# Performance work log

Measured on AMD Instinct MI355X. Metric: run time of the kernel, lower is better.

Reference implementation:

```python
import jax, jax.numpy as jnp
import numpy as np

TAU = 0.07
MARGIN = 0.2
NUM_SPECIES = 64  # matches fill_max of species_ids


def _l2norm(x):
    return x / jnp.linalg.norm(x, axis=-1, keepdims=True)


def setup_inputs() -> dict:
    key = jax.random.key(0)
    k1, k2, k3 = jax.random.split(key, 3)
    B, D = 8192, 256
    species_embed = _l2norm(jax.random.normal(k1, (B, D), dtype=jnp.float32))
    text_embed = _l2norm(jax.random.normal(k2, (B, D), dtype=jnp.float32))
    species_ids = jax.random.randint(k3, (B,), 0, NUM_SPECIES, dtype=jnp.int32)
    return {"species_embed": species_embed, "text_embed": text_embed,
            "species_ids": species_ids}


def reference(species_embed, text_embed, species_ids):
    B = species_embed.shape[0]
    dtype = species_embed.dtype

    sim = species_embed @ text_embed.T                      # (B, B)
    same = species_ids[:, None] == species_ids[None, :]     # (B, B) bool, symmetric
    diag_sim = jnp.diagonal(sim)                            # (B,)

    # ---- intra-species symmetric InfoNCE (per-species CE, averaged over species)
    logits = sim / TAU
    neg_inf = jnp.finfo(dtype).min
    masked = jnp.where(same, logits, neg_inf)               # restrict to same-species cols
    diag_logit = diag_sim / TAU
    ce_v2t = jax.scipy.special.logsumexp(masked, axis=1) - diag_logit   # per-row CE
    ce_t2v = jax.scipy.special.logsumexp(masked.T, axis=1) - diag_logit # transpose: same mask is symmetric

    ones = jnp.ones((B,), dtype=dtype)
    counts = jax.ops.segment_sum(ones, species_ids, num_segments=NUM_SPECIES)          # group sizes
    seg_v2t = jax.ops.segment_sum(ce_v2t, species_ids, num_segments=NUM_SPECIES)
    seg_t2v = jax.ops.segment_sum(ce_t2v, species_ids, num_segments=NUM_SPECIES)
    valid_s = counts >= 2                                   # groups with <2 members skipped
    per_species = (seg_v2t + seg_t2v) / (2.0 * jnp.maximum(counts, 1.0))
    n_valid = jnp.maximum(jnp.sum(valid_s.astype(dtype)), 1.0)
    loss_infonce = jnp.sum(jnp.where(valid_s, per_species, 0.0)) / n_valid

    # ---- cross-species triplet (pos = mean same-species sim excl. self, neg = mean diff-species sim)
    same_f = same.astype(dtype)
    row_same_sum = jnp.sum(sim * same_f, axis=1)            # includes diagonal
    row_sum = jnp.sum(sim, axis=1)
    pos_cnt = jnp.sum(same_f, axis=1) - 1.0
    neg_cnt = B - jnp.sum(same_f, axis=1)
    pos_mean = (row_same_sum - diag_sim) / jnp.maximum(pos_cnt, 1.0)
    neg_mean = (row_sum - row_same_sum) / jnp.maximum(neg_cnt, 1.0)
    tri = jax.nn.relu(neg_mean - pos_mean + MARGIN)
    valid_i = (pos_cnt > 0) & (neg_cnt > 0)
    n_valid_i = jnp.maximum(jnp.sum(valid_i.astype(dtype)), 1.0)
    loss_triplet = jnp.sum(jnp.where(valid_i, tri, 0.0)) / n_valid_i

    return loss_infonce + loss_triplet
```

## Files before the change

kernel.cpp:

```cpp
#include <hip/hip_runtime.h>
#include <hip/hip_fp16.h>

#define TAU 0.07f
#define MARGIN 0.2f
#define NSPEC 64
#define BB 8192
#define DD 256

#define WS_SCALARS   0
#define WS_COUNTS    288
#define WS_OFFSETS   544
#define WS_LSEROW    1024
#define WS_LSECOL    33792
#define WS_TS        66560
#define WS_DIAG      132096
#define WS_MEMBER    164864
#define WS_T         197632
#define WS_TRI       198656
#define WS_ZERO_BYTES 132096

typedef _Float16 half8 __attribute__((ext_vector_type(8)));
typedef float float4v __attribute__((ext_vector_type(4)));
typedef unsigned int uint4v __attribute__((ext_vector_type(4)));

__device__ __forceinline__ uint4v pack8(float4 a, float4 b) {
  half8 h;
  h[0] = (_Float16)a.x; h[1] = (_Float16)a.y; h[2] = (_Float16)a.z; h[3] = (_Float16)a.w;
  h[4] = (_Float16)b.x; h[5] = (_Float16)b.y; h[6] = (_Float16)b.z; h[7] = (_Float16)b.w;
  return __builtin_bit_cast(uint4v, h);
}

__global__ void k1_all(const int* __restrict__ ids, int* counts_g, int* offsets_g,
                       int* memberList, float* scalars) {
  __shared__ int cnt[NSPEC];
  __shared__ int off[NSPEC];
  int tid = threadIdx.x;
  if (tid < NSPEC) cnt[tid] = 0;
  __syncthreads();
  int myS[8], myP[8];
  #pragma unroll
  for (int r = 0; r < 8; ++r) {
    int i = r * 1024 + tid;
    int s = ids[i];
    myS[r] = s;
    myP[r] = atomicAdd(&cnt[s], 1);
  }
  __syncthreads();
  if (tid < NSPEC) {
    int o = 0;
    for (int t = 0; t < NSPEC; ++t) o += (t < tid) ? cnt[t] : 0;
    off[tid] = o;
    offsets_g[tid] = o;
    int c = cnt[tid];
    counts_g[tid] = c;
    unsigned long long bv = __ballot(c >= 2);
    float nvi = (c >= 2 && c <= BB - 1) ? (float)c : 0.f;
    for (int o2 = 1; o2 < 64; o2 <<= 1) nvi += __shfl_xor(nvi, o2);
    if (tid == 0) {
      scalars[2] = (float)__popcll(bv);
      scalars[3] = nvi;
    }
  }
  __syncthreads();
  #pragma unroll
  for (int r = 0; r < 8; ++r) {
    int i = r * 1024 + tid;
    memberList[off[myS[r]] + myP[r]] = i;
  }
}

__global__ void k2_ts(const float* __restrict__ tx, const int* __restrict__ counts,
                      const int* __restrict__ offsets, const int* __restrict__ memberList,
                      float* Ts) {
  int s = blockIdx.x, r = blockIdx.y;
  int m = counts[s], g0 = offsets[s];
  int k0 = (m * r) >> 3, k1 = (m * (r + 1)) >> 3;
  if (k0 >= k1) return;
  int d = threadIdx.x;
  float acc = 0.f;
  for (int k = k0; k < k1; ++k) acc += tx[memberList[g0 + k] * DD + d];
  atomicAdd(&Ts[s * DD + d], acc);
}

__global__ void k2b_t(const float* __restrict__ Ts, float* T) {
  int d = threadIdx.x;
  float acc = 0.f;
  for (int s = 0; s < NSPEC; ++s) acc += Ts[s * DD + d];
  T[d] = acc;
}

__global__ void k4_rows(const float* __restrict__ sp, const float* __restrict__ tx,
                        const int* __restrict__ ids, const int* __restrict__ counts,
                        const float* __restrict__ Ts, const float* __restrict__ T,
                        float* diag, float* tri) {
  int gt = blockIdx.x * 256 + threadIdx.x;
  int i = gt >> 6, lane = gt & 63;
  float4 a = *reinterpret_cast<const float4*>(sp + i * DD + lane * 4);
  float4 b = *reinterpret_cast<const float4*>(tx + i * DD + lane * 4);
  float4 tv = *reinterpret_cast<const float4*>(T + lane * 4);
  int s = ids[i];
  int m = counts[s];
  float4 c = *reinterpret_cast<const float4*>(Ts + s * DD + lane * 4);
  float dDiag = a.x * b.x + a.y * b.y + a.z * b.z + a.w * b.w;
  float dT    = a.x * tv.x + a.y * tv.y + a.z * tv.z + a.w * tv.w;
  float dTs   = a.x * c.x + a.y * c.y + a.z * c.z + a.w * c.w;
  #pragma unroll
  for (int o = 1; o < 64; o <<= 1) {
    dDiag += __shfl_xor(dDiag, o);
    dT    += __shfl_xor(dT, o);
    dTs   += __shfl_xor(dTs, o);
  }
  if (lane == 0) {
    diag[i] = dDiag;
    float posMean = (dTs - dDiag) / fmaxf((float)(m - 1), 1.f);
    float negMean = (dT - dTs) / fmaxf((float)(BB - m), 1.f);
    float t = fmaxf(negMean - posMean + MARGIN, 0.f);
    tri[i] = (m >= 2 && m <= BB - 1) ? t : 0.f;
  }
}

__global__ void k5_lse(const float* __restrict__ sp, const float* __restrict__ tx,
                       const int* __restrict__ counts, const int* __restrict__ offsets,
                       const int* __restrict__ memberList,
                       float* lseRow, float* lseCol) {
  __shared__ uint4v lds5[1536];
  int s = blockIdx.x;
  int m = counts[s];
  int g0 = offsets[s];
  int tid = threadIdx.x;
  int lane = tid & 63, wv = tid >> 6;
  int quad = lane >> 4, cl = lane & 15;

  for (int rt = blockIdx.y; rt * 64 < m; rt += gridDim.y) {
    for (int ct = blockIdx.z; ct * 128 < m; ct += gridDim.z) {
      float4v acc[8];
      #pragma unroll
      for (int cf = 0; cf < 8; ++cf) acc[cf] = (float4v){0.f, 0.f, 0.f, 0.f};

      for (int kc = 0; kc < 4; ++kc) {
        __syncthreads();
        #pragma unroll
        for (int p = 0; p < 6; ++p) {
          int u = p * 256 + tid;
          int isB = u >= 512;
          int v = isB ? (u - 512) : u;
          int row = v >> 3;
          int sub = v & 7;
          int ksl = sub >> 2, q = sub & 3;
          int d0 = kc * 64 + ksl * 32 + q * 8;
          int idx = isB ? (ct * 128 + row) : (rt * 64 + row);
          uint4v val = (uint4v){0u, 0u, 0u, 0u};
          if (idx < m) {
            const float* src = (isB ? tx : sp) + memberList[g0 + idx] * DD + d0;
            float4 f0 = *reinterpret_cast<const float4*>(src);
            float4 f1 = *reinterpret_cast<const float4*>(src + 4);
            val = pack8(f0, f1);
          }
          int dst = isB ? (512 + (ksl * 128 + row) * 4 + q)
                        : ((ksl * 64 + row) * 4 + q);
          lds5[dst] = val;
        }
        __syncthreads();
        #pragma unroll
        for (int ksl = 0; ksl < 2; ++ksl) {
          half8 a = __builtin_bit_cast(half8, lds5[(ksl * 64 + wv * 16 + cl) * 4 + quad]);
          #pragma unroll
          for (int cf = 0; cf < 8; ++cf) {
            half8 b = __builtin_bit_cast(half8, lds5[512 + (ksl * 128 + cf * 16 + cl) * 4 + quad]);
            acc[cf] = __builtin_amdgcn_mfma_f32_16x16x32_f16(a, b, acc[cf], 0, 0, 0);
          }
        }
      }

      int riBase = rt * 64 + wv * 16 + quad * 4;
      float rowAcc[4] = {0.f, 0.f, 0.f, 0.f};
      #pragma unroll
      for (int cf = 0; cf < 8; ++cf) {
        int ci = ct * 128 + cf * 16 + cl;
        bool cv = ci < m;
        float colAcc = 0.f;
        #pragma unroll
        for (int reg = 0; reg < 4; ++reg) {
          bool rv = (riBase + reg) < m;
          float e = (rv && cv) ? __expf(acc[cf][reg] * (1.f / TAU)) : 0.f;
          rowAcc[reg] += e;
          colAcc += e;
        }
        colAcc += __shfl_xor(colAcc, 16);
        colAcc += __shfl_xor(colAcc, 32);
        if (quad == 0 && cv) atomicAdd(&lseCol[g0 + ci], colAcc);
      }
      #pragma unroll
      for (int reg = 0; reg < 4; ++reg) {
        float v = rowAcc[reg];
        v += __shfl_xor(v, 1);
        v += __shfl_xor(v, 2);
        v += __shfl_xor(v, 4);
        v += __shfl_xor(v, 8);
        if (cl == 0 && (riBase + reg) < m) atomicAdd(&lseRow[g0 + riBase + reg], v);
      }
    }
  }
}

__global__ void k6_info(const int* __restrict__ memberList, const int* __restrict__ ids,
                        const int* __restrict__ counts, const float* __restrict__ lseRow,
                        const float* __restrict__ lseCol, const float* __restrict__ diag,
                        const float* __restrict__ tri, float* scalars) {
  __shared__ float red[8];
  int g = blockIdx.x * blockDim.x + threadIdx.x;
  int i = memberList[g];
  int s = ids[i];
  int m = counts[s];
  float tt = tri[i];
  float term = 0.f;
  if (m >= 2) {
    term = (__logf(lseRow[g]) + __logf(lseCol[g]) - 2.f * diag[i] * (1.f / TAU)) /
           (2.f * (float)m);
  }
  #pragma unroll
  for (int o = 1; o < 64; o <<= 1) {
    term += __shfl_xor(term, o);
    tt += __shfl_xor(tt, o);
  }
  int wv = threadIdx.x >> 6, lane = threadIdx.x & 63;
  if (lane == 0) { red[wv] = term; red[4 + wv] = tt; }
  __syncthreads();
  if (threadIdx.x == 0) {
    atomicAdd(&scalars[1], red[0] + red[1] + red[2] + red[3]);
    atomicAdd(&scalars[0], red[4] + red[5] + red[6] + red[7]);
  }
}

__global__ void k7_final(const float* __restrict__ scalars, float* out) {
  out[0] = scalars[1] / fmaxf(scalars[2], 1.f) + scalars[0] / fmaxf(scalars[3], 1.f);
}

extern "C" void kernel_launch(void* const* d_in, const int* in_sizes, int n_in,
                              void* d_out, int out_size, void* d_ws, size_t ws_size,
                              hipStream_t stream) {
  const float* sp = (const float*)d_in[0];
  const float* tx = (const float*)d_in[1];
  const int* ids = (const int*)d_in[2];
  float* out = (float*)d_out;

  char* ws = (char*)d_ws;
  float* scalars = (float*)(ws + WS_SCALARS);
  int* counts = (int*)(ws + WS_COUNTS);
  int* offsets = (int*)(ws + WS_OFFSETS);
  float* lseRow = (float*)(ws + WS_LSEROW);
  float* lseCol = (float*)(ws + WS_LSECOL);
  float* Ts = (float*)(ws + WS_TS);
  float* diag = (float*)(ws + WS_DIAG);
  int* memberList = (int*)(ws + WS_MEMBER);
  float* T = (float*)(ws + WS_T);
  float* tri = (float*)(ws + WS_TRI);

  hipMemsetAsync(d_ws, 0, WS_ZERO_BYTES, stream);
  k1_all<<<1, 1024, 0, stream>>>(ids, counts, offsets, memberList, scalars);
  k2_ts<<<dim3(NSPEC, 8), 256, 0, stream>>>(tx, counts, offsets, memberList, Ts);
  k2b_t<<<1, 256, 0, stream>>>(Ts, T);
  k4_rows<<<BB / 4, 256, 0, stream>>>(sp, tx, ids, counts, Ts, T, diag, tri);
  k5_lse<<<dim3(NSPEC, 4, 2), 256, 0, stream>>>(sp, tx, counts, offsets, memberList,
                                                lseRow, lseCol);
  k6_info<<<32, 256, 0, stream>>>(memberList, ids, counts, lseRow, lseCol, diag, tri,
                                  scalars);
  k7_final<<<1, 1, 0, stream>>>(scalars, out);
}
```

Before: 111.1 us.

## Fuse launches: zero workspace in k1, fold T reduction and row stats into k6

Removes the memset, k2b_t, k4_rows and k7_final launches. Workspace zeroing moves into k1_all, the global T reduction is done by a single block of k5_lse, the per-row diag and triplet dot products move into the final reduction kernel, and the last block (tracked by an atomic counter) writes the output. The goal is to cut launch count and the diag/tri intermediate traffic. In exchange, k1 now zeroes about 132KB with a single block, and correctness relies on the designated k5 block writing T before k6 runs, which holds through stream ordering.

Measured after the change: 119.5 us. 1.08x slower.

```diff
diff --git a/kernel.cpp b/kernel.cpp
--- a/kernel.cpp
+++ b/kernel.cpp
@@ -13,11 +13,9 @@
 #define WS_LSEROW    1024
 #define WS_LSECOL    33792
 #define WS_TS        66560
-#define WS_DIAG      132096
-#define WS_MEMBER    164864
-#define WS_T         197632
-#define WS_TRI       198656
-#define WS_ZERO_BYTES 132096
+#define WS_T         132096
+#define WS_MEMBER    133120
+#define ZERO_F4      8256
 
 typedef _Float16 half8 __attribute__((ext_vector_type(8)));
 typedef float float4v __attribute__((ext_vector_type(4)));
@@ -31,10 +29,13 @@
 }
 
 __global__ void k1_all(const int* __restrict__ ids, int* counts_g, int* offsets_g,
-                       int* memberList, float* scalars) {
+                       int* memberList, float* scalars, float4v* zb) {
   __shared__ int cnt[NSPEC];
   __shared__ int off[NSPEC];
   int tid = threadIdx.x;
+  float4v z4 = {0.f, 0.f, 0.f, 0.f};
+  for (int u = tid; u < ZERO_F4; u += 1024) zb[u] = z4;
+  if (tid < 8) ((unsigned*)scalars)[tid] = 0u;
   if (tid < NSPEC) cnt[tid] = 0;
   __syncthreads();
   int myS[8], myP[8];
@@ -82,47 +83,19 @@
   atomicAdd(&Ts[s * DD + d], acc);
 }
 
-__global__ void k2b_t(const float* __restrict__ Ts, float* T) {
-  int d = threadIdx.x;
-  float acc = 0.f;
-  for (int s = 0; s < NSPEC; ++s) acc += Ts[s * DD + d];
-  T[d] = acc;
-}
-
-__global__ void k4_rows(const float* __restrict__ sp, const float* __restrict__ tx,
-                        const int* __restrict__ ids, const int* __restrict__ counts,
-                        const float* __restrict__ Ts, const float* __restrict__ T,
-                        float* diag, float* tri) {
-  int gt = blockIdx.x * 256 + threadIdx.x;
-  int i = gt >> 6, lane = gt & 63;
-  float4 a = *reinterpret_cast<const float4*>(sp + i * DD + lane * 4);
-  float4 b = *reinterpret_cast<const float4*>(tx + i * DD + lane * 4);
-  float4 tv = *reinterpret_cast<const float4*>(T + lane * 4);
-  int s = ids[i];
-  int m = counts[s];
-  float4 c = *reinterpret_cast<const float4*>(Ts + s * DD + lane * 4);
-  float dDiag = a.x * b.x + a.y * b.y + a.z * b.z + a.w * b.w;
-  float dT    = a.x * tv.x + a.y * tv.y + a.z * tv.z + a.w * tv.w;
-  float dTs   = a.x * c.x + a.y * c.y + a.z * c.z + a.w * c.w;
-  #pragma unroll
-  for (int o = 1; o < 64; o <<= 1) {
-    dDiag += __shfl_xor(dDiag, o);
-    dT    += __shfl_xor(dT, o);
-    dTs   += __shfl_xor(dTs, o);
-  }
-  if (lane == 0) {
-    diag[i] = dDiag;
-    float posMean = (dTs - dDiag) / fmaxf((float)(m - 1), 1.f);
-    float negMean = (dT - dTs) / fmaxf((float)(BB - m), 1.f);
-    float t = fmaxf(negMean - posMean + MARGIN, 0.f);
-    tri[i] = (m >= 2 && m <= BB - 1) ? t : 0.f;
-  }
-}
-
 __global__ void k5_lse(const float* __restrict__ sp, const float* __restrict__ tx,
                        const int* __restrict__ counts, const int* __restrict__ offsets,
                        const int* __restrict__ memberList,
+                       const float* __restrict__ Ts, float* T,
                        float* lseRow, float* lseCol) {
+  if (blockIdx.x == 0 && blockIdx.y == 3 && blockIdx.z == 1) {
+    int d = threadIdx.x;
+    float acc = 0.f;
+    #pragma unroll
+    for (int s = 0; s < NSPEC; ++s) acc += Ts[s * DD + d];
+    T[d] = acc;
+  }
+
   __shared__ uint4v lds5[1536];
   int s = blockIdx.x;
   int m = counts[s];
@@ -203,37 +176,62 @@
   }
 }
 
-__global__ void k6_info(const int* __restrict__ memberList, const int* __restrict__ ids,
-                        const int* __restrict__ counts, const float* __restrict__ lseRow,
-                        const float* __restrict__ lseCol, const float* __restrict__ diag,
-                        const float* __restrict__ tri, float* scalars) {
-  __shared__ float red[8];
-  int g = blockIdx.x * blockDim.x + threadIdx.x;
+__global__ void k6_fused(const float* __restrict__ sp, const float* __restrict__ tx,
+                         const int* __restrict__ ids, const int* __restrict__ counts,
+                         const int* __restrict__ memberList,
+                         const float* __restrict__ Ts, const float* __restrict__ T,
+                         const float* __restrict__ lseRow, const float* __restrict__ lseCol,
+                         float* scalars, float* out) {
+  __shared__ float red[32];
+  int tid = threadIdx.x;
+  int gt = blockIdx.x * 1024 + tid;
+  int g = gt >> 6, lane = gt & 63;
   int i = memberList[g];
   int s = ids[i];
   int m = counts[s];
-  float tt = tri[i];
-  float term = 0.f;
-  if (m >= 2) {
-    term = (__logf(lseRow[g]) + __logf(lseCol[g]) - 2.f * diag[i] * (1.f / TAU)) /
-           (2.f * (float)m);
-  }
+  float4 a = *reinterpret_cast<const float4*>(sp + i * DD + lane * 4);
+  float4 b = *reinterpret_cast<const float4*>(tx + i * DD + lane * 4);
+  float4 c = *reinterpret_cast<const float4*>(Ts + s * DD + lane * 4);
+  float4 tv = *reinterpret_cast<const float4*>(T + lane * 4);
+  float dDiag = a.x * b.x + a.y * b.y + a.z * b.z + a.w * b.w;
+  float dTs   = a.x * c.x + a.y * c.y + a.z * c.z + a.w * c.w;
+  float dT    = a.x * tv.x + a.y * tv.y + a.z * tv.z + a.w * tv.w;
   #pragma unroll
   for (int o = 1; o < 64; o <<= 1) {
-    term += __shfl_xor(term, o);
-    tt += __shfl_xor(tt, o);
-  }
-  int wv = threadIdx.x >> 6, lane = threadIdx.x & 63;
-  if (lane == 0) { red[wv] = term; red[4 + wv] = tt; }
-  __syncthreads();
-  if (threadIdx.x == 0) {
-    atomicAdd(&scalars[1], red[0] + red[1] + red[2] + red[3]);
-    atomicAdd(&scalars[0], red[4] + red[5] + red[6] + red[7]);
-  }
-}
-
-__global__ void k7_final(const float* __restrict__ scalars, float* out) {
-  out[0] = scalars[1] / fmaxf(scalars[2], 1.f) + scalars[0] / fmaxf(scalars[3], 1.f);
+    dDiag += __shfl_xor(dDiag, o);
+    dTs   += __shfl_xor(dTs, o);
+    dT    += __shfl_xor(dT, o);
+  }
+  if (lane == 0) {
+    float term = 0.f, tri = 0.f;
+    if (m >= 2) {
+      term = (__logf(lseRow[g]) + __logf(lseCol[g]) - 2.f * dDiag * (1.f / TAU)) /
+             (2.f * (float)m);
+      float posMean = (dTs - dDiag) / fmaxf((float)(m - 1), 1.f);
+      float negMean = (dT - dTs) / fmaxf((float)(BB - m), 1.f);
+      if (m <= BB - 1) tri = fmaxf(negMean - posMean + MARGIN, 0.f);
+    }
+    int wv = tid >> 6;
+    red[wv] = term;
+    red[16 + wv] = tri;
+  }
+  __syncthreads();
+  if (tid == 0) {
+    float infoS = 0.f, triS = 0.f;
+    #pragma unroll
+    for (int w = 0; w < 16; ++w) { infoS += red[w]; triS += red[16 + w]; }
+    atomicAdd(&scalars[1], infoS);
+    atomicAdd(&scalars[0], triS);
+    __threadfence();
+    unsigned prev = atomicAdd((unsigned*)&scalars[4], 1u);
+    if (prev == gridDim.x - 1) {
+      float fi = atomicAdd(&scalars[1], 0.f);
+      float ft = atomicAdd(&scalars[0], 0.f);
+      float nv = scalars[2];
+      float nvi = scalars[3];
+      out[0] = fi / fmaxf(nv, 1.f) + ft / fmaxf(nvi, 1.f);
+    }
+  }
 }
 
 extern "C" void kernel_launch(void* const* d_in, const int* in_sizes, int n_in,
@@ -251,19 +249,14 @@
   float* lseRow = (float*)(ws + WS_LSEROW);
   float* lseCol = (float*)(ws + WS_LSECOL);
   float* Ts = (float*)(ws + WS_TS);
-  float* diag = (float*)(ws + WS_DIAG);
+  float* T = (float*)(ws + WS_T);
   int* memberList = (int*)(ws + WS_MEMBER);
-  float* T = (float*)(ws + WS_T);
-  float* tri = (float*)(ws + WS_TRI);
-
-  hipMemsetAsync(d_ws, 0, WS_ZERO_BYTES, stream);
-  k1_all<<<1, 1024, 0, stream>>>(ids, counts, offsets, memberList, scalars);
+
+  k1_all<<<1, 1024, 0, stream>>>(ids, counts, offsets, memberList, scalars,
+                                 (float4v*)(ws + WS_LSEROW));
   k2_ts<<<dim3(NSPEC, 8), 256, 0, stream>>>(tx, counts, offsets, memberList, Ts);
-  k2b_t<<<1, 256, 0, stream>>>(Ts, T);
-  k4_rows<<<BB / 4, 256, 0, stream>>>(sp, tx, ids, counts, Ts, T, diag, tri);
   k5_lse<<<dim3(NSPEC, 4, 2), 256, 0, stream>>>(sp, tx, counts, offsets, memberList,
-                                                lseRow, lseCol);
-  k6_info<<<32, 256, 0, stream>>>(memberList, ids, counts, lseRow, lseCol, diag, tri,
-                                  scalars);
-  k7_final<<<1, 1, 0, stream>>>(scalars, out);
-}
+                                                Ts, T, lseRow, lseCol);
+  k6_fused<<<BB / 16, 1024, 0, stream>>>(sp, tx, ids, counts, memberList, Ts, T,
+                                         lseRow, lseCol, scalars, out);
+}
```
